# Kernel optimization log

Hardware: AMD Instinct MI355X
Metric: run time of the kernel (lower is better)

The kernel has to match this reference:

```python
import jax, jax.numpy as jnp
import numpy as np

N = 50000
IN_DIM = 128
HID = 64
HEADS = 4
OUT_DIM = 2
NEG_SLOPE = 0.2


def setup_inputs() -> dict:
    key = jax.random.key(0)
    ks = jax.random.split(key, 10)
    x = jax.random.normal(ks[0], (N, IN_DIM), dtype=jnp.float32)
    edge_index = jax.random.randint(ks[1], (2, 800000), 0, N, dtype=jnp.int64)
    s = 0.1
    W1 = jax.random.normal(ks[2], (IN_DIM, HEADS * HID), dtype=jnp.float32) * s
    att_src1 = jax.random.normal(ks[3], (HEADS, HID), dtype=jnp.float32) * s
    att_dst1 = jax.random.normal(ks[4], (HEADS, HID), dtype=jnp.float32) * s
    b1 = jnp.zeros((HEADS * HID,), dtype=jnp.float32)
    W2 = jax.random.normal(ks[5], (HEADS * HID, 1 * OUT_DIM), dtype=jnp.float32) * s
    att_src2 = jax.random.normal(ks[6], (1, OUT_DIM), dtype=jnp.float32) * s
    att_dst2 = jax.random.normal(ks[7], (1, OUT_DIM), dtype=jnp.float32) * s
    b2 = jnp.zeros((OUT_DIM,), dtype=jnp.float32)
    return {"x": x, "edge_index": edge_index, "W1": W1, "att_src1": att_src1,
            "att_dst1": att_dst1, "b1": b1, "W2": W2, "att_src2": att_src2,
            "att_dst2": att_dst2, "b2": b2}


def gat_conv(x, W, att_src, att_dst, b, src, dst, heads, ch):
    # x: [N, F_in] -> h: [N, H, C]
    n = x.shape[0]
    h = (x @ W).reshape(n, heads, ch)
    a_s = jnp.einsum('nhc,hc->nh', h, att_src)  # [N, H]
    a_d = jnp.einsum('nhc,hc->nh', h, att_dst)  # [N, H]
    e = jax.nn.leaky_relu(a_s[src] + a_d[dst], NEG_SLOPE)  # [E, H]
    # segment softmax over incoming edges of each destination node
    m = jax.ops.segment_max(e, dst, num_segments=n)
    ex = jnp.exp(e - m[dst])
    z = jax.ops.segment_sum(ex, dst, num_segments=n)
    alpha = ex / z[dst]  # [E, H]
    msg = h[src] * alpha[:, :, None]  # [E, H, C]
    out = jax.ops.segment_sum(msg, dst, num_segments=n)  # [N, H, C]
    return out.reshape(n, heads * ch) + b


def reference(x, edge_index, W1, att_src1, att_dst1, b1, W2, att_src2, att_dst2, b2):
    n = x.shape[0]
    loop = jnp.arange(n, dtype=edge_index.dtype)
    src = jnp.concatenate([edge_index[0], loop])  # add_self_loops (PyG default)
    dst = jnp.concatenate([edge_index[1], loop])
    h = gat_conv(x, W1, att_src1, att_dst1, b1, src, dst, HEADS, HID)
    h = jax.nn.elu(h)
    # dropout is identity at inference
    out = gat_conv(h, W2, att_src2, att_dst2, b2, src, dst, 1, OUT_DIM)
    return out
```

## Files before the change

kernel.cpp:

```cpp
#include <hip/hip_runtime.h>

#define NN     50000
#define E_RAW  800000
#define ETOT   (E_RAW + NN)
#define FIN    128
#define FH     256
#define NEG    0.2f
#define BCAP   64
#define GEMM_NB ((NN + 63) / 64)
#define SC_NB   ((ETOT + 255) / 256)

typedef __attribute__((ext_vector_type(8))) short s16x8;
typedef __attribute__((ext_vector_type(4))) float f32x4;

static __device__ __forceinline__ float leaky(float v) { return v > 0.f ? v : NEG * v; }

static __device__ __forceinline__ unsigned short f2bf(float f) {
    unsigned u = __float_as_uint(f);
    unsigned r = u + 0x7fffu + ((u >> 16) & 1u);
    return (unsigned short)(r >> 16);
}

__global__ __launch_bounds__(256) void k_prep(const float* __restrict__ W1,
                                              unsigned short* __restrict__ Wt_bf,
                                              int* __restrict__ cnt)
{
    const int b = blockIdx.x, t = threadIdx.x;
    if (b < FIN) Wt_bf[t * FIN + b] = f2bf(W1[b * FH + t]);
    int idx = b * 256 + t;
    if (idx < NN) cnt[idx] = 0;
}

__global__ __launch_bounds__(256) void k_gx(const float* __restrict__ x,
                                            const unsigned short* __restrict__ Wt_bf,
                                            const float* __restrict__ att_src,
                                            const float* __restrict__ att_dst,
                                            const int* __restrict__ ei,
                                            int* __restrict__ cnt,
                                            int* __restrict__ csr_src,
                                            unsigned short* __restrict__ h1b,
                                            float* __restrict__ a_s,
                                            float* __restrict__ a_d)
{
    const int t = threadIdx.x;

    if (blockIdx.x >= GEMM_NB) {
        const int e = (blockIdx.x - GEMM_NB) * 256 + t;
        if (e >= ETOT) return;
        int s, d;
        if (e < E_RAW) { s = ei[e]; d = ei[E_RAW + e]; } else { s = e - E_RAW; d = s; }
        int pos = atomicAdd(&cnt[d], 1);
        if (pos >= BCAP) return;
        csr_src[(d << 6) + pos] = s;
        return;
    }

    __shared__ unsigned short Sbuf[64 * 256];
    const int w    = t >> 6;
    const int lane = t & 63;
    const int li   = lane & 15;
    const int q8   = (lane >> 4) * 8;
    const int quad = lane >> 4;
    const int n0   = blockIdx.x * 64;

    {
        const int node_l = t >> 2;
        const int k0 = (t & 3) * 32;
        int nn = n0 + node_l; if (nn >= NN) nn = NN - 1;
        const float* xp = &x[(size_t)nn * FIN + k0];
        unsigned short* xd = &Sbuf[node_l * 136 + k0];
#pragma unroll
        for (int i = 0; i < 8; i++) {
            float4 v = *(const float4*)&xp[i * 4];
            xd[i * 4 + 0] = f2bf(v.x);
            xd[i * 4 + 1] = f2bf(v.y);
            xd[i * 4 + 2] = f2bf(v.z);
            xd[i * 4 + 3] = f2bf(v.w);
        }
    }
    __syncthreads();

    f32x4 acc[4][4];
#pragma unroll
    for (int i = 0; i < 4; i++)
#pragma unroll
        for (int j = 0; j < 4; j++) acc[i][j] = (f32x4){0.f, 0.f, 0.f, 0.f};

#pragma unroll
    for (int kki = 0; kki < 4; kki++) {
        const int kk = kki * 32;
        s16x8 af[4], bf[4];
#pragma unroll
        for (int n16 = 0; n16 < 4; n16++) {
            int col = w * 64 + n16 * 16 + li;
            bf[n16] = *(const s16x8*)&Wt_bf[col * FIN + kk + q8];
        }
#pragma unroll
        for (int m16 = 0; m16 < 4; m16++)
            af[m16] = *(const s16x8*)&Sbuf[(m16 * 16 + li) * 136 + kk + q8];
#pragma unroll
        for (int m16 = 0; m16 < 4; m16++)
#pragma unroll
            for (int n16 = 0; n16 < 4; n16++)
                acc[m16][n16] = __builtin_amdgcn_mfma_f32_16x16x32_bf16(
                    af[m16], bf[n16], acc[m16][n16], 0, 0, 0);
    }

    {
        float as_c[4], ad_c[4];
#pragma unroll
        for (int n16 = 0; n16 < 4; n16++) {
            int col = w * 64 + n16 * 16 + li;
            as_c[n16] = att_src[col];
            ad_c[n16] = att_dst[col];
        }
#pragma unroll
        for (int m16 = 0; m16 < 4; m16++) {
            float ps[4], pd[4];
#pragma unroll
            for (int reg = 0; reg < 4; reg++) {
                float s = 0.f, d = 0.f;
#pragma unroll
                for (int n16 = 0; n16 < 4; n16++) {
                    s += acc[m16][n16][reg] * as_c[n16];
                    d += acc[m16][n16][reg] * ad_c[n16];
                }
                ps[reg] = s; pd[reg] = d;
            }
#pragma unroll
            for (int off = 1; off < 16; off <<= 1) {
#pragma unroll
                for (int reg = 0; reg < 4; reg++) {
                    ps[reg] += __shfl_xor(ps[reg], off);
                    pd[reg] += __shfl_xor(pd[reg], off);
                }
            }
            if (li == 0) {
#pragma unroll
                for (int reg = 0; reg < 4; reg++) {
                    int node = n0 + m16 * 16 + quad * 4 + reg;
                    if (node < NN) {
                        a_s[node * 4 + w] = ps[reg];
                        a_d[node * 4 + w] = pd[reg];
                    }
                }
            }
        }
    }

    __syncthreads();
#pragma unroll
    for (int m16 = 0; m16 < 4; m16++)
#pragma unroll
        for (int n16 = 0; n16 < 4; n16++)
#pragma unroll
            for (int reg = 0; reg < 4; reg++)
                Sbuf[(m16 * 16 + quad * 4 + reg) * FH + w * 64 + n16 * 16 + li] =
                    f2bf(acc[m16][n16][reg]);
    __syncthreads();
    {
        const int node_l = t >> 2;
        const int c0 = (t & 3) * 64;
        int node = n0 + node_l;
        if (node < NN) {
#pragma unroll
            for (int i = 0; i < 8; i++)
                *(uint4*)&h1b[(size_t)node * FH + c0 + i * 8] =
                    *(const uint4*)&Sbuf[node_l * FH + c0 + i * 8];
        }
    }
}

__global__ __launch_bounds__(256) void k_agg1(const int* __restrict__ cnt,
                                              const int* __restrict__ csr_src,
                                              const float* __restrict__ a_s1,
                                              const float* __restrict__ a_d1,
                                              const unsigned short* __restrict__ h1b,
                                              const float* __restrict__ b1,
                                              const float* __restrict__ W2,
                                              const float* __restrict__ att_src2,
                                              const float* __restrict__ att_dst2,
                                              float4* __restrict__ nd4)
{
    const int lane = threadIdx.x & 63;
    const int n = blockIdx.x * 4 + (threadIdx.x >> 6);
    if (n >= NN) return;
    int m = cnt[n]; if (m > BCAP) m = BCAP;
    const int base = n << 6;
    const int h = lane >> 4;
    const float ad_h = a_d1[n * 4 + h];
    float acc0 = 0.f, acc1 = 0.f, acc2 = 0.f, acc3 = 0.f, z = 0.f;
    const int* sp = &csr_src[base];
#pragma unroll 4
    for (int j = 0; j < m; j++) {
        int s = sp[j];
        float as_h = a_s1[s * 4 + h];
        float ex = __expf(leaky(as_h + ad_h));
        unsigned long long wv =
            *(const unsigned long long*)(h1b + (size_t)s * FH + lane * 4);
        unsigned lo = (unsigned)wv, hi = (unsigned)(wv >> 32);
        acc0 += __uint_as_float(lo << 16) * ex;
        acc1 += __uint_as_float(lo & 0xffff0000u) * ex;
        acc2 += __uint_as_float(hi << 16) * ex;
        acc3 += __uint_as_float(hi & 0xffff0000u) * ex;
        z += ex;
    }
    const int c0 = lane * 4;
    float4 bb = *(const float4*)&b1[c0];
    float v0 = acc0 / z + bb.x;
    float v1 = acc1 / z + bb.y;
    float v2 = acc2 / z + bb.z;
    float v3 = acc3 / z + bb.w;
    v0 = v0 > 0.f ? v0 : __expf(v0) - 1.f;
    v1 = v1 > 0.f ? v1 : __expf(v1) - 1.f;
    v2 = v2 > 0.f ? v2 : __expf(v2) - 1.f;
    v3 = v3 > 0.f ? v3 : __expf(v3) - 1.f;
    float4 w2a = *(const float4*)&W2[c0 * 2];
    float4 w2b = *(const float4*)&W2[c0 * 2 + 4];
    float s0 = v0 * w2a.x + v1 * w2a.z + v2 * w2b.x + v3 * w2b.z;
    float s1 = v0 * w2a.y + v1 * w2a.w + v2 * w2b.y + v3 * w2b.w;
#pragma unroll
    for (int off = 32; off; off >>= 1) {
        s0 += __shfl_xor(s0, off);
        s1 += __shfl_xor(s1, off);
    }
    if (lane == 0) {
        float4 nd;
        nd.x = s0; nd.y = s1;
        nd.z = s0 * att_src2[0] + s1 * att_src2[1];
        nd.w = s0 * att_dst2[0] + s1 * att_dst2[1];
        nd4[n] = nd;
    }
}

__global__ __launch_bounds__(256) void k_agg2(const int* __restrict__ cnt,
                                              const int* __restrict__ csr_src,
                                              const float4* __restrict__ nd4,
                                              const float* __restrict__ b2,
                                              float* __restrict__ out)
{
    const int l = threadIdx.x & 15;
    const int n = blockIdx.x * 16 + (threadIdx.x >> 4);
    if (n >= NN) return;
    int m = cnt[n]; if (m > BCAP) m = BCAP;
    const int base = n << 6;
    const float ad = nd4[n].w;
    float z = 0.f, a0 = 0.f, a1 = 0.f;
    for (int j = l; j < m; j += 16) {
        int s = csr_src[base + j];
        float4 f = nd4[s];
        float ex = __expf(leaky(f.z + ad));
        z  += ex;
        a0 += f.x * ex;
        a1 += f.y * ex;
    }
#pragma unroll
    for (int off = 8; off; off >>= 1) {
        z  += __shfl_xor(z, off);
        a0 += __shfl_xor(a0, off);
        a1 += __shfl_xor(a1, off);
    }
    if (l == 0) {
        out[n * 2 + 0] = a0 / z + b2[0];
        out[n * 2 + 1] = a1 / z + b2[1];
    }
}

extern "C" void kernel_launch(void* const* d_in, const int* in_sizes, int n_in,
                              void* d_out, int out_size, void* d_ws, size_t ws_size,
                              hipStream_t stream)
{
    const float* x        = (const float*)d_in[0];
    const int*   ei       = (const int*)d_in[1];
    const float* W1       = (const float*)d_in[2];
    const float* att_src1 = (const float*)d_in[3];
    const float* att_dst1 = (const float*)d_in[4];
    const float* b1       = (const float*)d_in[5];
    const float* W2       = (const float*)d_in[6];
    const float* att_src2 = (const float*)d_in[7];
    const float* att_dst2 = (const float*)d_in[8];
    const float* b2       = (const float*)d_in[9];
    float* out = (float*)d_out;

    int*    csr_src = (int*)d_ws;
    unsigned short* h1b = (unsigned short*)(csr_src + (size_t)NN * BCAP);
    unsigned short* Wt_bf = h1b + (size_t)NN * FH;
    int*    cnt   = (int*)(Wt_bf + FH * FIN);
    float*  a_s1  = (float*)(cnt + NN);
    float*  a_d1  = a_s1 + (size_t)NN * 4;
    float4* nd4   = (float4*)(a_d1 + (size_t)NN * 4);

    k_prep<<<200, 256, 0, stream>>>(W1, Wt_bf, cnt);
    k_gx<<<GEMM_NB + SC_NB, 256, 0, stream>>>(x, Wt_bf, att_src1, att_dst1, ei,
                                              cnt, csr_src, h1b, a_s1, a_d1);
    k_agg1<<<(NN + 3) / 4, 256, 0, stream>>>(cnt, csr_src, a_s1, a_d1, h1b,
                                             b1, W2, att_src2, att_dst2, nd4);
    k_agg2<<<(NN + 15) / 16, 256, 0, stream>>>(cnt, csr_src, nd4, b2, out);
}
```

Baseline: 233.3 us.

## Replace global-atomic edge scatter with LDS-partitioned bucketed CSR build

Edge bucketing moves from global atomics on a per-node counter to LDS atomics. Each workgroup owns a slice of destination nodes and scans a quarter of the edges, writing into a per-replica sub-bucket of 32 slots, so each node has 4 sub-buckets of 128 slots in total. Self-loops are written directly, and the W1 transpose is folded into the same kernel. This also separates the scatter from the GEMM, and the aggregation kernels loop over 4 sub-buckets. The cost is 64 workgroups that each scan 200k edges, which gives low parallelism and a lot of redundant reads of the edge array, plus a larger CSR footprint.

```diff
diff --git a/kernel.cpp b/kernel.cpp
--- a/kernel.cpp
+++ b/kernel.cpp
@@ -6,9 +6,15 @@
 #define FIN    128
 #define FH     256
 #define NEG    0.2f
-#define BCAP   64
+
+#define P_PART 16
+#define DPW    3125
+#define R_REP  4
+#define EPW    (E_RAW / R_REP)
+#define SCAT_WGS (P_PART * R_REP)
+#define PREP_WGS 8
+#define BSUB   32
 #define GEMM_NB ((NN + 63) / 64)
-#define SC_NB   ((ETOT + 255) / 256)
 
 typedef __attribute__((ext_vector_type(8))) short s16x8;
 typedef __attribute__((ext_vector_type(4))) float f32x4;
@@ -21,41 +27,60 @@
     return (unsigned short)(r >> 16);
 }
 
-__global__ __launch_bounds__(256) void k_prep(const float* __restrict__ W1,
-                                              unsigned short* __restrict__ Wt_bf,
-                                              int* __restrict__ cnt)
-{
-    const int b = blockIdx.x, t = threadIdx.x;
-    if (b < FIN) Wt_bf[t * FIN + b] = f2bf(W1[b * FH + t]);
-    int idx = b * 256 + t;
-    if (idx < NN) cnt[idx] = 0;
-}
-
-__global__ __launch_bounds__(256) void k_gx(const float* __restrict__ x,
-                                            const unsigned short* __restrict__ Wt_bf,
-                                            const float* __restrict__ att_src,
-                                            const float* __restrict__ att_dst,
-                                            const int* __restrict__ ei,
-                                            int* __restrict__ cnt,
-                                            int* __restrict__ csr_src,
-                                            unsigned short* __restrict__ h1b,
-                                            float* __restrict__ a_s,
-                                            float* __restrict__ a_d)
+__global__ __launch_bounds__(1024) void k_scat(const int* __restrict__ ei,
+                                               const float* __restrict__ W1,
+                                               unsigned short* __restrict__ Wt_bf,
+                                               int* __restrict__ cnt,
+                                               int* __restrict__ csr_src)
 {
     const int t = threadIdx.x;
-
-    if (blockIdx.x >= GEMM_NB) {
-        const int e = (blockIdx.x - GEMM_NB) * 256 + t;
-        if (e >= ETOT) return;
-        int s, d;
-        if (e < E_RAW) { s = ei[e]; d = ei[E_RAW + e]; } else { s = e - E_RAW; d = s; }
-        int pos = atomicAdd(&cnt[d], 1);
-        if (pos >= BCAP) return;
-        csr_src[(d << 6) + pos] = s;
+    if (blockIdx.x >= SCAT_WGS) {
+        const int base = (blockIdx.x - SCAT_WGS) * 4096;
+        for (int i = t; i < 4096; i += 1024) {
+            int idx = base + i;
+            int k = idx >> 8, col = idx & 255;
+            Wt_bf[col * FIN + k] = f2bf(W1[k * FH + col]);
+        }
         return;
     }
-
+    __shared__ int lcnt[DPW];
+    const int p  = blockIdx.x >> 2;
+    const int r  = blockIdx.x & 3;
+    const int lo = p * DPW;
+    for (int i = t; i < DPW; i += 1024) {
+        lcnt[i] = (r == 0) ? 1 : 0;
+        if (r == 0) csr_src[(size_t)(lo + i) << 7] = lo + i;
+    }
+    __syncthreads();
+    const int ebase = r * EPW, eend = ebase + EPW;
+    for (int e0 = ebase + t * 4; e0 < eend; e0 += 4096) {
+        int4 dv = *(const int4*)&ei[E_RAW + e0];
+#pragma unroll
+        for (int k = 0; k < 4; k++) {
+            int d = (&dv.x)[k];
+            unsigned rel = (unsigned)(d - lo);
+            if (rel < DPW) {
+                int pos = atomicAdd(&lcnt[rel], 1);
+                if (pos < BSUB)
+                    csr_src[((size_t)d << 7) + (r << 5) + pos] = ei[e0 + k];
+            }
+        }
+    }
+    __syncthreads();
+    for (int i = t; i < DPW; i += 1024)
+        cnt[(lo + i) * 4 + r] = lcnt[i];
+}
+
+__global__ __launch_bounds__(256) void k_gemm1(const float* __restrict__ x,
+                                               const unsigned short* __restrict__ Wt_bf,
+                                               const float* __restrict__ att_src,
+                                               const float* __restrict__ att_dst,
+                                               unsigned short* __restrict__ h1b,
+                                               float* __restrict__ a_s,
+                                               float* __restrict__ a_d)
+{
     __shared__ unsigned short Sbuf[64 * 256];
+    const int t    = threadIdx.x;
     const int w    = t >> 6;
     const int lane = t & 63;
     const int li   = lane & 15;
@@ -185,25 +210,28 @@
     const int lane = threadIdx.x & 63;
     const int n = blockIdx.x * 4 + (threadIdx.x >> 6);
     if (n >= NN) return;
-    int m = cnt[n]; if (m > BCAP) m = BCAP;
-    const int base = n << 6;
+    int4 c4 = *(const int4*)&cnt[n * 4];
     const int h = lane >> 4;
     const float ad_h = a_d1[n * 4 + h];
     float acc0 = 0.f, acc1 = 0.f, acc2 = 0.f, acc3 = 0.f, z = 0.f;
-    const int* sp = &csr_src[base];
+#pragma unroll
+    for (int r = 0; r < 4; r++) {
+        int mr = (&c4.x)[r]; if (mr > BSUB) mr = BSUB;
+        const int* sp = &csr_src[((size_t)n << 7) + (r << 5)];
 #pragma unroll 4
-    for (int j = 0; j < m; j++) {
-        int s = sp[j];
-        float as_h = a_s1[s * 4 + h];
-        float ex = __expf(leaky(as_h + ad_h));
-        unsigned long long wv =
-            *(const unsigned long long*)(h1b + (size_t)s * FH + lane * 4);
-        unsigned lo = (unsigned)wv, hi = (unsigned)(wv >> 32);
-        acc0 += __uint_as_float(lo << 16) * ex;
-        acc1 += __uint_as_float(lo & 0xffff0000u) * ex;
-        acc2 += __uint_as_float(hi << 16) * ex;
-        acc3 += __uint_as_float(hi & 0xffff0000u) * ex;
-        z += ex;
+        for (int j = 0; j < mr; j++) {
+            int s = sp[j];
+            float as_h = a_s1[s * 4 + h];
+            float ex = __expf(leaky(as_h + ad_h));
+            unsigned long long wv =
+                *(const unsigned long long*)(h1b + (size_t)s * FH + lane * 4);
+            unsigned lo = (unsigned)wv, hi = (unsigned)(wv >> 32);
+            acc0 += __uint_as_float(lo << 16) * ex;
+            acc1 += __uint_as_float(lo & 0xffff0000u) * ex;
+            acc2 += __uint_as_float(hi << 16) * ex;
+            acc3 += __uint_as_float(hi & 0xffff0000u) * ex;
+            z += ex;
+        }
     }
     const int c0 = lane * 4;
     float4 bb = *(const float4*)&b1[c0];
@@ -242,17 +270,21 @@
     const int l = threadIdx.x & 15;
     const int n = blockIdx.x * 16 + (threadIdx.x >> 4);
     if (n >= NN) return;
-    int m = cnt[n]; if (m > BCAP) m = BCAP;
-    const int base = n << 6;
+    int4 c4 = *(const int4*)&cnt[n * 4];
     const float ad = nd4[n].w;
     float z = 0.f, a0 = 0.f, a1 = 0.f;
-    for (int j = l; j < m; j += 16) {
-        int s = csr_src[base + j];
-        float4 f = nd4[s];
-        float ex = __expf(leaky(f.z + ad));
-        z  += ex;
-        a0 += f.x * ex;
-        a1 += f.y * ex;
+#pragma unroll
+    for (int r = 0; r < 4; r++) {
+        int mr = (&c4.x)[r]; if (mr > BSUB) mr = BSUB;
+        const int* sp = &csr_src[((size_t)n << 7) + (r << 5)];
+        for (int j = l; j < mr; j += 16) {
+            int s = sp[j];
+            float4 f = nd4[s];
+            float ex = __expf(leaky(f.z + ad));
+            z  += ex;
+            a0 += f.x * ex;
+            a1 += f.y * ex;
+        }
     }
 #pragma unroll
     for (int off = 8; off; off >>= 1) {
@@ -283,16 +315,15 @@
     float* out = (float*)d_out;
 
     int*    csr_src = (int*)d_ws;
-    unsigned short* h1b = (unsigned short*)(csr_src + (size_t)NN * BCAP);
+    unsigned short* h1b = (unsigned short*)(csr_src + (size_t)NN * 128);
     unsigned short* Wt_bf = h1b + (size_t)NN * FH;
     int*    cnt   = (int*)(Wt_bf + FH * FIN);
-    float*  a_s1  = (float*)(cnt + NN);
+    float*  a_s1  = (float*)(cnt + (size_t)NN * 4);
     float*  a_d1  = a_s1 + (size_t)NN * 4;
     float4* nd4   = (float4*)(a_d1 + (size_t)NN * 4);
 
-    k_prep<<<200, 256, 0, stream>>>(W1, Wt_bf, cnt);
-    k_gx<<<GEMM_NB + SC_NB, 256, 0, stream>>>(x, Wt_bf, att_src1, att_dst1, ei,
-                                              cnt, csr_src, h1b, a_s1, a_d1);
+    k_scat<<<SCAT_WGS + PREP_WGS, 1024, 0, stream>>>(ei, W1, Wt_bf, cnt, csr_src);
+    k_gemm1<<<GEMM_NB, 256, 0, stream>>>(x, Wt_bf, att_src1, att_dst1, h1b, a_s1, a_d1);
     k_agg1<<<(NN + 3) / 4, 256, 0, stream>>>(cnt, csr_src, a_s1, a_d1, h1b,
                                              b1, W2, att_src2, att_dst2, nd4);
     k_agg2<<<(NN + 15) / 16, 256, 0, stream>>>(cnt, csr_src, nd4, b2, out);
```

Result: slower. 266.4 us (+14.2%).
